# Kernel optimization log

Hardware: AMD Instinct MI355X
Metric: run time of the kernel (lower is better)

The kernel has to match this reference:

```python
import jax, jax.numpy as jnp
import numpy as np

K = 4
TEMPERATURE = 30.0


def setup_inputs() -> dict:
    key = jax.random.key(0)
    ks = jax.random.split(key, 6)
    B, C, H, W_sp = 32, 128, 56, 56
    Cout, kh, kw = 128, 3, 3
    Cred = max(C // 4, 1)
    x = jax.random.normal(ks[0], (B, C, H, W_sp), dtype=jnp.float32)
    # K parallel conv kernels + biases (fan-in scaled init)
    fan = C * kh * kw
    W = jax.random.normal(ks[1], (K, Cout, C, kh, kw), dtype=jnp.float32) / np.sqrt(fan)
    b = jax.random.normal(ks[2], (K, Cout), dtype=jnp.float32) * 0.01
    # attention branch: 1x1 convs == dense on pooled features
    aw1 = jax.random.normal(ks[3], (Cred, C), dtype=jnp.float32) / np.sqrt(C)
    aw2 = jax.random.normal(ks[4], (K, Cred), dtype=jnp.float32) / np.sqrt(Cred)
    return {"x": x, "W": W, "b": b, "aw1": aw1, "aw2": aw2}


def reference(x, W, b, aw1, aw2):
    # attention: global avg pool -> 1x1 conv (dense) -> relu -> 1x1 conv -> softmax(logits/T)
    pooled = jnp.mean(x, axis=(2, 3))                       # [B, C]
    h1 = jax.nn.relu(jnp.einsum('bc,rc->br', pooled, aw1))  # [B, Cred]
    logits = jnp.einsum('br,kr->bk', h1, aw2)               # [B, K]
    attn = jax.nn.softmax(logits / TEMPERATURE, axis=1)     # [B, K]

    pad = 1
    out = None
    for i in range(K):  # fixed small K, structurally distinct kernels
        yi = jax.lax.conv_general_dilated(
            x, W[i], window_strides=(1, 1), padding=[(pad, pad), (pad, pad)],
            dimension_numbers=('NCHW', 'OIHW', 'NCHW'))
        yi = yi + b[i][None, :, None, None]
        yi = yi * attn[:, i][:, None, None, None]
        out = yi if out is None else out + yi
    return out
```

## Files before the change

### kernel.cpp

```cpp
#include <hip/hip_runtime.h>
#include <hip/hip_bf16.h>
#include <stdint.h>

typedef __bf16 bf16x8 __attribute__((ext_vector_type(8)));
typedef float  f32x4  __attribute__((ext_vector_type(4)));
typedef unsigned short u16x8 __attribute__((ext_vector_type(8)));

#define NB 32
#define NC 128
#define NH 56
#define NW 56
#define NK 4
#define NCO 128
#define NCR 32
#define NHW 3136
#define TEMPER 30.0f

#define WS_ATTN   0u
#define WS_BC     4096u
#define WS_ROWSUM 65536u
#define WS_WC     1048576u
#define WS_XT     10485760u

__global__ void xt_kernel(const float* __restrict__ x, __hip_bfloat16* __restrict__ xt,
                          float* __restrict__ rowsum) {
  __shared__ float lds[58 * 133];
  int xcd = blockIdx.x & 7;
  int j   = blockIdx.x >> 3;
  int b   = xcd * 4 + j / 58;
  int hp  = j % 58;
  int blk = b * 58 + hp;
  int h = hp - 1;
  bool hin = (h >= 0) && (h < NH);
  int tid = threadIdx.x;
  if (hin) {
    const float* xrow = x + ((size_t)b * NC) * NHW + (size_t)h * NW;
    for (int i = tid; i < 128 * 14; i += 256) {
      int c = i / 14;
      int w4 = (i - c * 14) * 4;
      float4 v = *(const float4*)(xrow + (size_t)c * NHW + w4);
      int base = (w4 + 1) * 133 + c;
      lds[base]         = v.x;
      lds[base + 133]   = v.y;
      lds[base + 2*133] = v.z;
      lds[base + 3*133] = v.w;
    }
  }
  __syncthreads();
  __hip_bfloat16* orow = xt + (size_t)blk * (58 * 128);
  for (int i = tid; i < 58 * 16; i += 256) {
    int wp = i >> 4;
    int cg = (i & 15) << 3;
    u16x8 o;
    if (!hin || wp == 0 || wp == 57) {
      o = (u16x8)0;
    } else {
      const float* src = lds + wp * 133 + cg;
      #pragma unroll
      for (int jx = 0; jx < 8; ++jx) {
        union { __hip_bfloat16 b; unsigned short u; } cv;
        cv.b = __float2bfloat16(src[jx]);
        o[jx] = cv.u;
      }
    }
    *(u16x8*)(orow + wp * 128 + cg) = o;
  }
  if (hin && tid < 128) {
    float s = 0.f;
    #pragma unroll 8
    for (int wp = 1; wp <= 56; ++wp) s += lds[wp * 133 + tid];
    rowsum[(size_t)blk * 128 + tid] = s;
  }
}

__global__ void attn_kernel(const float* __restrict__ rowsum, const float* __restrict__ aw1,
                            const float* __restrict__ aw2, const float* __restrict__ bias,
                            float* __restrict__ attn, float* __restrict__ bc_out) {
  int b = blockIdx.x;
  __shared__ float sp[NC], h1[NCR], at[NK];
  int t = threadIdx.x;
  if (t < NC) {
    float s = 0.f;
    for (int hp = 1; hp <= 56; ++hp) s += rowsum[((size_t)b * 58 + hp) * 128 + t];
    sp[t] = s * (1.0f / (float)NHW);
  }
  __syncthreads();
  if (t < NCR) {
    float s = 0.f;
    for (int c = 0; c < NC; ++c) s += aw1[t*NC + c] * sp[c];
    h1[t] = s > 0.f ? s : 0.f;
  }
  __syncthreads();
  if (t == 0) {
    float lg[NK], mx = -1e30f;
    for (int k = 0; k < NK; ++k) {
      float s = 0.f;
      for (int r = 0; r < NCR; ++r) s += aw2[k*NCR + r] * h1[r];
      lg[k] = s * (1.0f/TEMPER);
      mx = fmaxf(mx, lg[k]);
    }
    float den = 0.f, e[NK];
    for (int k = 0; k < NK; ++k) { e[k] = expf(lg[k]-mx); den += e[k]; }
    float inv = 1.0f/den;
    for (int k = 0; k < NK; ++k) { at[k] = e[k]*inv; attn[b*NK+k] = at[k]; }
  }
  __syncthreads();
  if (t < NCO) {
    float s = 0.f;
    for (int k = 0; k < NK; ++k) s += at[k] * bias[k*NCO + t];
    bc_out[b*NCO + t] = s;
  }
}

__global__ void combine_kernel(const float* __restrict__ W, const float* __restrict__ attn,
                               __hip_bfloat16* __restrict__ wc) {
  int gid = blockIdx.x;
  int bg  = gid >> 6;
  int tcell = (gid & 63) * 256 + threadIdx.x;
  int co = tcell >> 7, ci = tcell & 127;
  float w[4][9];
  const float* wp = W + ((size_t)co * 128 + ci) * 9;
  #pragma unroll
  for (int k = 0; k < 4; ++k)
    #pragma unroll
    for (int j = 0; j < 9; ++j)
      w[k][j] = wp[(size_t)k * 147456 + j];
  for (int b = bg * 8; b < bg * 8 + 8; ++b) {
    float a0 = attn[b*4+0], a1 = attn[b*4+1], a2 = attn[b*4+2], a3 = attn[b*4+3];
    #pragma unroll
    for (int j = 0; j < 9; ++j) {
      float v = a0*w[0][j] + a1*w[1][j] + a2*w[2][j] + a3*w[3][j];
      wc[(((size_t)b*9 + j) * 128 + co) * 128 + ci] = __float2bfloat16(v);
    }
  }
}

#define RS 2368
#define CS 40
#define BCHP 1280
#define ACH 1536

#define GLOAD16(src, dst) \
  __builtin_amdgcn_global_load_lds( \
    (const __attribute__((address_space(1))) unsigned int*)(src), \
    (__attribute__((address_space(3))) unsigned int*)(dst), 16, 0, 0)

__global__ __launch_bounds__(256, 3) void conv_kernel(
    const unsigned short* __restrict__ xt,
    const unsigned short* __restrict__ wc,
    const float* __restrict__ bc,
    float* __restrict__ out) {
  __shared__ __align__(16) unsigned short lds_b[BCHP*8];
  __shared__ __align__(16) unsigned short lds_a[ACH*8];
  const int tid  = threadIdx.x;
  const int lane = tid & 63;
  const int wm   = tid >> 6;
  const int bid  = blockIdx.x;
  const int xcd  = bid & 7;
  const int jj   = bid >> 3;
  const int b    = xcd*4 + jj/28;
  const int r0   = (jj % 28) * 2;
  const int li   = lane & 15;
  const int kg   = lane >> 4;

  int srcB[5];
  #pragma unroll
  for (int i = 0; i < 5; ++i) {
    int q = i*256 + tid;
    int r = q / 296;
    int sl = q - r*296;
    int col = sl / 5;
    int part = sl - col*5;
    int rc = r > 3 ? 3 : r;
    int cl = col > 57 ? 57 : col;
    int pc = part > 3 ? 3 : part;
    srcB[i] = ((r0 + rc)*58 + cl)*128 + pc*8;
  }
  int srcA[6];
  #pragma unroll
  for (int i = 0; i < 6; ++i) {
    int c = i*256 + tid;
    int khwL = c >> 9;
    int co   = (c & 511) >> 2;
    int part = c & 3;
    srcA[i] = (khwL*128 + co)*128 + part*8;
  }

  int xoff[7];
  #pragma unroll
  for (int f = 0; f < 7; ++f) {
    int pos = f*16 + li;
    int rB = pos / 56;
    int cB = pos - rB*56;
    xoff[f] = rB*RS + cB*CS + kg*8;
  }
  const int aRead = (wm*32 + li)*32 + kg*8;

  const f32x4 vzero = {0.f, 0.f, 0.f, 0.f};
  f32x4 acc[2][7];
  #pragma unroll
  for (int mo = 0; mo < 2; ++mo)
    #pragma unroll
    for (int f = 0; f < 7; ++f) acc[mo][f] = vzero;

  const unsigned short* xtg = xt + (size_t)b*(58*58*128);
  const unsigned short* wcg = wc + (size_t)b*(9*128*128);

  for (int cc = 0; cc < 4; ++cc) {
    #pragma unroll
    for (int kh = 0; kh < 3; ++kh) {
      __syncthreads();
      #pragma unroll
      for (int i = 0; i < 6; ++i)
        GLOAD16(wcg + kh*49152 + srcA[i] + cc*32, lds_a + (i*256 + wm*64)*8);
      if (kh == 0) {
        #pragma unroll
        for (int i = 0; i < 5; ++i)
          GLOAD16(xtg + srcB[i] + cc*32, lds_b + (i*256 + wm*64)*8);
      }
      __syncthreads();
      #pragma unroll
      for (int kwl = 0; kwl < 3; ++kwl) {
        bf16x8 af[2];
        #pragma unroll
        for (int mo = 0; mo < 2; ++mo)
          af[mo] = *(const bf16x8*)(lds_a + kwl*4096 + aRead + mo*512);
        bf16x8 bfr[7];
        #pragma unroll
        for (int f = 0; f < 7; ++f)
          bfr[f] = *(const bf16x8*)(lds_b + xoff[f] + kh*RS + kwl*CS);
        #pragma unroll
        for (int mo = 0; mo < 2; ++mo)
          #pragma unroll
          for (int f = 0; f < 7; ++f)
            acc[mo][f] = __builtin_amdgcn_mfma_f32_16x16x32_bf16(af[mo], bfr[f], acc[mo][f], 0, 0, 0);
      }
    }
  }

  float* ob = out + (size_t)b*NCO*NHW;
  #pragma unroll
  for (int mo = 0; mo < 2; ++mo) {
    #pragma unroll
    for (int rg = 0; rg < 4; ++rg) {
      const int co = wm*32 + mo*16 + kg*4 + rg;
      const float bv = bc[b*NCO + co];
      float* orow = ob + (size_t)co*NHW;
      #pragma unroll
      for (int f = 0; f < 7; ++f) {
        int pos = f*16 + li;
        int rB = pos / 56;
        int cB = pos - rB*56;
        orow[(r0 + rB)*56 + cB] = acc[mo][f][rg] + bv;
      }
    }
  }
}

extern "C" void kernel_launch(void* const* d_in, const int* in_sizes, int n_in,
                              void* d_out, int out_size, void* d_ws, size_t ws_size,
                              hipStream_t stream) {
  const float* x   = (const float*)d_in[0];
  const float* W   = (const float*)d_in[1];
  const float* bia = (const float*)d_in[2];
  const float* aw1 = (const float*)d_in[3];
  const float* aw2 = (const float*)d_in[4];
  float* out = (float*)d_out;
  char* ws = (char*)d_ws;
  float* attn   = (float*)(ws + WS_ATTN);
  float* bcm    = (float*)(ws + WS_BC);
  float* rowsum = (float*)(ws + WS_ROWSUM);
  __hip_bfloat16* wc = (__hip_bfloat16*)(ws + WS_WC);
  __hip_bfloat16* xt = (__hip_bfloat16*)(ws + WS_XT);

  xt_kernel<<<NB*58, 256, 0, stream>>>(x, xt, rowsum);
  attn_kernel<<<NB, 128, 0, stream>>>(rowsum, aw1, aw2, bia, attn, bcm);
  combine_kernel<<<256, 256, 0, stream>>>(W, attn, wc);
  conv_kernel<<<896, 256, 0, stream>>>((const unsigned short*)xt,
                                       (const unsigned short*)wc, bcm, out);
}
```

Before: 71.57 us.

## Enlarge conv tile to 4 rows with 2x2 wave grid and padded weight LDS

Each conv block now computes four output rows instead of two, with waves split 2x2 over output channels and pixels, so each wave holds a 64x112 accumulator tile. Weights are loaded through registers into a padded LDS layout (stride 40) to reduce bank conflicts, replacing direct global-to-LDS loads. This halves the grid and raises per-block reuse of weight tiles, at the cost of doubled accumulator registers, lower occupancy (launch bounds 2), and only 448 blocks for the machine.

```diff
diff --git a/kernel.cpp b/kernel.cpp
--- a/kernel.cpp
+++ b/kernel.cpp
@@ -5,6 +5,7 @@
 typedef __bf16 bf16x8 __attribute__((ext_vector_type(8)));
 typedef float  f32x4  __attribute__((ext_vector_type(4)));
 typedef unsigned short u16x8 __attribute__((ext_vector_type(8)));
+typedef unsigned int   u32x4 __attribute__((ext_vector_type(4)));
 
 #define NB 32
 #define NC 128
@@ -137,69 +138,72 @@
 
 #define RS 2368
 #define CS 40
-#define BCHP 1280
-#define ACH 1536
+#define ACS 40
+#define AKWS (128*ACS)
 
 #define GLOAD16(src, dst) \
   __builtin_amdgcn_global_load_lds( \
     (const __attribute__((address_space(1))) unsigned int*)(src), \
     (__attribute__((address_space(3))) unsigned int*)(dst), 16, 0, 0)
 
-__global__ __launch_bounds__(256, 3) void conv_kernel(
+__global__ __launch_bounds__(256, 2) void conv_kernel(
     const unsigned short* __restrict__ xt,
     const unsigned short* __restrict__ wc,
     const float* __restrict__ bc,
     float* __restrict__ out) {
-  __shared__ __align__(16) unsigned short lds_b[BCHP*8];
-  __shared__ __align__(16) unsigned short lds_a[ACH*8];
+  __shared__ __align__(16) unsigned short lds_b[1792*8];
+  __shared__ __align__(16) unsigned short lds_a[3*AKWS];
   const int tid  = threadIdx.x;
   const int lane = tid & 63;
-  const int wm   = tid >> 6;
+  const int wv   = tid >> 6;
+  const int wm   = wv & 1;
+  const int wn   = wv >> 1;
   const int bid  = blockIdx.x;
   const int xcd  = bid & 7;
   const int jj   = bid >> 3;
-  const int b    = xcd*4 + jj/28;
-  const int r0   = (jj % 28) * 2;
+  const int b    = xcd*4 + jj/14;
+  const int r0   = (jj % 14) * 4;
   const int li   = lane & 15;
   const int kg   = lane >> 4;
 
-  int srcB[5];
-  #pragma unroll
-  for (int i = 0; i < 5; ++i) {
+  int srcB[7];
+  #pragma unroll
+  for (int i = 0; i < 7; ++i) {
     int q = i*256 + tid;
     int r = q / 296;
     int sl = q - r*296;
     int col = sl / 5;
     int part = sl - col*5;
-    int rc = r > 3 ? 3 : r;
+    int rc = r > 5 ? 5 : r;
     int cl = col > 57 ? 57 : col;
     int pc = part > 3 ? 3 : part;
     srcB[i] = ((r0 + rc)*58 + cl)*128 + pc*8;
   }
-  int srcA[6];
+  int srcA[6], dstA[6];
   #pragma unroll
   for (int i = 0; i < 6; ++i) {
     int c = i*256 + tid;
-    int khwL = c >> 9;
+    int kwl  = c >> 9;
     int co   = (c & 511) >> 2;
     int part = c & 3;
-    srcA[i] = (khwL*128 + co)*128 + part*8;
+    srcA[i] = (kwl*128 + co)*128 + part*8;
+    dstA[i] = kwl*AKWS + co*ACS + part*8;
   }
 
   int xoff[7];
   #pragma unroll
   for (int f = 0; f < 7; ++f) {
-    int pos = f*16 + li;
+    int pos = wn*112 + f*16 + li;
     int rB = pos / 56;
     int cB = pos - rB*56;
     xoff[f] = rB*RS + cB*CS + kg*8;
   }
-  const int aRead = (wm*32 + li)*32 + kg*8;
+  const int aRead = (wm*64 + li)*ACS + kg*8;
 
   const f32x4 vzero = {0.f, 0.f, 0.f, 0.f};
-  f32x4 acc[2][7];
-  #pragma unroll
-  for (int mo = 0; mo < 2; ++mo)
+  f32x4 acc[4][7];
+  #pragma unroll
+  for (int mo = 0; mo < 4; ++mo)
     #pragma unroll
     for (int f = 0; f < 7; ++f) acc[mo][f] = vzero;
 
@@ -209,28 +213,32 @@
   for (int cc = 0; cc < 4; ++cc) {
     #pragma unroll
     for (int kh = 0; kh < 3; ++kh) {
+      u32x4 areg[6];
+      #pragma unroll
+      for (int i = 0; i < 6; ++i)
+        areg[i] = *(const u32x4*)(wcg + kh*49152 + srcA[i] + cc*32);
       __syncthreads();
+      if (kh == 0) {
+        #pragma unroll
+        for (int i = 0; i < 7; ++i)
+          GLOAD16(xtg + srcB[i] + cc*32, lds_b + (i*256 + wv*64)*8);
+      }
       #pragma unroll
       for (int i = 0; i < 6; ++i)
-        GLOAD16(wcg + kh*49152 + srcA[i] + cc*32, lds_a + (i*256 + wm*64)*8);
-      if (kh == 0) {
-        #pragma unroll
-        for (int i = 0; i < 5; ++i)
-          GLOAD16(xtg + srcB[i] + cc*32, lds_b + (i*256 + wm*64)*8);
-      }
+        *(u32x4*)(lds_a + dstA[i]) = areg[i];
       __syncthreads();
       #pragma unroll
       for (int kwl = 0; kwl < 3; ++kwl) {
-        bf16x8 af[2];
-        #pragma unroll
-        for (int mo = 0; mo < 2; ++mo)
-          af[mo] = *(const bf16x8*)(lds_a + kwl*4096 + aRead + mo*512);
+        bf16x8 af[4];
+        #pragma unroll
+        for (int mo = 0; mo < 4; ++mo)
+          af[mo] = *(const bf16x8*)(lds_a + kwl*AKWS + aRead + mo*(16*ACS));
         bf16x8 bfr[7];
         #pragma unroll
         for (int f = 0; f < 7; ++f)
           bfr[f] = *(const bf16x8*)(lds_b + xoff[f] + kh*RS + kwl*CS);
         #pragma unroll
-        for (int mo = 0; mo < 2; ++mo)
+        for (int mo = 0; mo < 4; ++mo)
           #pragma unroll
           for (int f = 0; f < 7; ++f)
             acc[mo][f] = __builtin_amdgcn_mfma_f32_16x16x32_bf16(af[mo], bfr[f], acc[mo][f], 0, 0, 0);
@@ -240,15 +248,15 @@
 
   float* ob = out + (size_t)b*NCO*NHW;
   #pragma unroll
-  for (int mo = 0; mo < 2; ++mo) {
+  for (int mo = 0; mo < 4; ++mo) {
     #pragma unroll
     for (int rg = 0; rg < 4; ++rg) {
-      const int co = wm*32 + mo*16 + kg*4 + rg;
+      const int co = wm*64 + mo*16 + kg*4 + rg;
       const float bv = bc[b*NCO + co];
       float* orow = ob + (size_t)co*NHW;
       #pragma unroll
       for (int f = 0; f < 7; ++f) {
-        int pos = f*16 + li;
+        int pos = wn*112 + f*16 + li;
         int rB = pos / 56;
         int cB = pos - rB*56;
         orow[(r0 + rB)*56 + cB] = acc[mo][f][rg] + bv;
@@ -276,6 +284,6 @@
   xt_kernel<<<NB*58, 256, 0, stream>>>(x, xt, rowsum);
   attn_kernel<<<NB, 128, 0, stream>>>(rowsum, aw1, aw2, bia, attn, bcm);
   combine_kernel<<<256, 256, 0, stream>>>(W, attn, wc);
-  conv_kernel<<<896, 256, 0, stream>>>((const unsigned short*)xt,
+  conv_kernel<<<448, 256, 0, stream>>>((const unsigned short*)xt,
                                        (const unsigned short*)wc, bcm, out);
 }
```

New measurement: 66.26 us. -7.4%, faster.
